# Kernel tuning notes

Hardware: AMD Instinct MI355X
Metric: run time of the kernel (lower is better)

## Reference

```python
import jax, jax.numpy as jnp
import numpy as np

_ANCHORS_PX = np.array([[116,90],[156,198],[373,326],
                        [30,61],[62,45],[59,119],
                        [10,13],[16,30],[33,23]], dtype=np.float32)
IMG = 416.0
NORMD_ANCHORS = jnp.asarray(_ANCHORS_PX / IMG)  # [9,2] normalized (w,h)
CLASSES = 80
LAMBDA_CLASS = 5.0


def _build_targets(targets, F, start):
    # targets: [B,N,5] = (cx,cy,w,h,cls), normalized coords.
    # Vectorized version of the per-box Python loop: IoU-match every box
    # against all 9 anchors (boxes pinned at origin, so IoU = wh overlap),
    # keep boxes whose best anchor belongs to this pyramid level, scatter
    B, N, _ = targets.shape
    C = CLASSES
    cx, cy, w, h = targets[..., 0], targets[..., 1], targets[..., 2], targets[..., 3]
    cls = targets[..., 4].astype(jnp.int32)
    fx, fy = cx * F, cy * F
    gx = jnp.floor(fx).astype(jnp.int32)
    gy = jnp.floor(fy).astype(jnp.int32)
    tx, ty = fx - gx, fy - gy
    aw_all, ah_all = NORMD_ANCHORS[:, 0], NORMD_ANCHORS[:, 1]
    # origin-pinned IoU: inter = min(w,aw)*min(h,ah)
    inter = jnp.minimum(w[..., None], aw_all) * jnp.minimum(h[..., None], ah_all)  # [B,N,9]
    union = (w * h)[..., None] + aw_all * ah_all - inter
    best = jnp.argmax(inter / union, axis=-1)                     # [B,N]
    assigned = (best >= start) & (best < start + 3)
    a = (best % 3).astype(jnp.int32)
    aw = jnp.take(aw_all, best)
    ah = jnp.take(ah_all, best)
    tw = jnp.log(w / aw)
    th = jnp.log(h / ah)
    b = jnp.arange(B, dtype=jnp.int32)[:, None]
    size = B * 3 * F * F
    flat = ((b * 3 + a) * F + gy) * F + gx                        # [B,N]
    flat = jnp.where(assigned, flat, size).reshape(-1)            # OOB -> dropped

    def scat(vals, init=0.0):
        buf = jnp.full((size,), init, dtype=jnp.float32)
        return buf.at[flat].set(vals.reshape(-1), mode='drop').reshape(B, 3, F, F)

    ones = jnp.ones((B, N), jnp.float32)
    t_x, t_y = scat(tx), scat(ty)
    t_w, t_h = scat(tw), scat(th)
    lw_xw, lw_yh = scat(w), scat(h)
    obj = scat(ones)
    noobj = scat(jnp.zeros((B, N), jnp.float32), init=1.0)
    flatc = flat * C + cls.reshape(-1)                            # OOB stays OOB
    cls_t = jnp.zeros((size * C,), jnp.float32).at[flatc].set(1.0, mode='drop')
    cls_t = cls_t.reshape(B, 3, F, F, C)
    return t_x, t_y, t_w, t_h, lw_xw, lw_yh, obj, cls_t, noobj


def _bce_mean(z, t):
    # torch BCELoss(sigmoid(z), t) with default mean reduction, written stably
    return jnp.mean(-(t * jax.nn.log_sigmoid(z) + (1.0 - t) * jax.nn.log_sigmoid(-z)))


def _level_loss(feat, targets, start):
    B, _, F, _ = feat.shape
    C = CLASSES
    t_x, t_y, t_w, t_h, lw_xw, lw_yh, obj, cls_t, noobj = _build_targets(targets, F, start)
    f = feat.reshape(B, 3, 5 + C, F, F).transpose(0, 1, 3, 4, 2)  # [B,3,F,F,5+C]
    zx, zy = f[..., 0], f[..., 1]
    pw, ph = f[..., 2], f[..., 3]
    zc = f[..., 4]
    zcls = f[..., 5:]
    scale = 2.0 - lw_xw * lw_yh
    # NOTE: original multiplies the scalar mean-reduced BCE/MSE by the mask
    # tensor and sums -> scalar_mean * sum(weights). Reproduced faithfully.
    loss_x = _bce_mean(zx, t_x) * jnp.sum(scale * obj)
    loss_y = _bce_mean(zy, t_y) * jnp.sum(scale * obj)
    loss_w = jnp.mean((pw - t_w) ** 2) * jnp.sum(0.5 * scale * obj)
    loss_h = jnp.mean((ph - t_h) ** 2) * jnp.sum(0.5 * scale * obj)
    bce_c = _bce_mean(zc, obj)
    loss_conf = bce_c * jnp.sum(obj) + bce_c * jnp.sum(noobj)     # lambda_obj=lambda_noobj=1
    # class loss: mean BCE over cells where obj==1 (boolean-mask mean in torch)
    bce_cls = -(cls_t * jax.nn.log_sigmoid(zcls) + (1.0 - cls_t) * jax.nn.log_sigmoid(-zcls))
    n_obj = jnp.sum(obj)
    loss_class = jnp.sum(bce_cls * obj[..., None]) / (n_obj * C)
    loss = loss_x + loss_y + loss_w + loss_h + loss_conf + LAMBDA_CLASS * loss_class
    return loss, n_obj


def setup_inputs() -> dict:
    key = jax.random.key(0)
    k1, k2, k3, k4 = jax.random.split(key, 4)
    B, N, C = 64, 50, CLASSES
    p13 = 0.1 * jax.random.normal(k1, (B, 3 * (5 + C), 13, 13), jnp.float32)
    p26 = 0.1 * jax.random.normal(k2, (B, 3 * (5 + C), 26, 26), jnp.float32)
    p52 = 0.1 * jax.random.normal(k3, (B, 3 * (5 + C), 52, 52), jnp.float32)
    kxy, kwh, kc = jax.random.split(k4, 3)
    cxcy = jax.random.uniform(kxy, (B, N, 2), jnp.float32, 0.01, 0.99)
    wh = jax.random.uniform(kwh, (B, N, 2), jnp.float32, 0.02, 0.9)
    cls = jax.random.randint(kc, (B, N, 1), 0, C).astype(jnp.float32)
    targets = jnp.concatenate([cxcy, wh, cls], axis=-1)  # [B,N,5]
    return {"predict_13": p13, "predict_26": p26, "predict_52": p52, "targets": targets}


def reference(predict_13, predict_26, predict_52, targets):
    l13, n13 = _level_loss(predict_13, targets, 0)
    l26, n26 = _level_loss(predict_26, targets, 3)
    l52, n52 = _level_loss(predict_52, targets, 6)
    return (l13 + l26 + l52) / (n13 + n26 + n52)
```

## Files before the change

kernel.cpp:

```cpp
#include <hip/hip_runtime.h>

#define NB 64
#define NT 50
#define NC 80

#define S13 (NB*3*13*13)
#define S26 (NB*3*26*26)
#define S52 (NB*3*52*52)

#define PB_BLOCKS 256
#define DN_BLOCKS 768
#define NBLK (PB_BLOCKS + DN_BLOCKS)

__device__ float g_partT[48][NBLK];

#define A_SPX 0
#define A_SPY 1
#define A_SW2 2
#define A_SH2 3
#define A_SPC 4
#define A_TXZ 5
#define A_TYZ 6
#define A_TW  7
#define A_TH  8
#define A_ZC  9
#define A_SSC 10
#define A_NOB 11
#define A_CSP 12
#define A_CZ  13

__device__ __forceinline__ float softplusf(float z){
    return fmaxf(z, 0.f) + __logf(1.f + __expf(-fabsf(z)));
}

struct TDec {
    int lvl, a, gx, gy, F, FF, off;
    float tx, ty, tw, th, w, h;
    int cls;
};

__device__ __forceinline__ TDec decode_target(const float* __restrict__ tgt, int b, int n){
    const float aw[9] = {116.f/416.f,156.f/416.f,373.f/416.f, 30.f/416.f, 62.f/416.f,
                          59.f/416.f, 10.f/416.f, 16.f/416.f, 33.f/416.f};
    const float ah[9] = { 90.f/416.f,198.f/416.f,326.f/416.f, 61.f/416.f, 45.f/416.f,
                         119.f/416.f, 13.f/416.f, 30.f/416.f, 23.f/416.f};
    const float* t = tgt + (b*NT + n)*5;
    float cx = t[0], cy = t[1], w = t[2], h = t[3];
    TDec d;
    d.cls = (int)t[4];
    d.w = w; d.h = h;
    float wh = w*h;
    int best = 0; float bi = -1.f, baw = aw[0], bah = ah[0];
    #pragma unroll
    for (int k = 0; k < 9; ++k){
        float inter = fminf(w, aw[k]) * fminf(h, ah[k]);
        float uni   = wh + aw[k]*ah[k] - inter;
        float r     = inter / uni;
        if (r > bi){ bi = r; best = k; baw = aw[k]; bah = ah[k]; }
    }
    d.lvl = best / 3;
    d.a   = best - d.lvl*3;
    d.F   = (d.lvl==0) ? 13 : (d.lvl==1 ? 26 : 52);
    d.FF  = d.F * d.F;
    d.off = (d.lvl==0) ? 0 : (d.lvl==1 ? S13 : (S13+S26));
    float fx = cx * (float)d.F, fy = cy * (float)d.F;
    d.gx = (int)floorf(fx); d.gy = (int)floorf(fy);
    d.tx = fx - (float)d.gx; d.ty = fy - (float)d.gy;
    d.tw = logf(w / baw);
    d.th = logf(h / bah);
    return d;
}

template<int FF, int LVL>
__device__ __forceinline__ void dense_scalar(const float* __restrict__ feat, int gb, float* sacc){
    constexpr int elems = NB*3*5*FF;
    constexpr int cFF = 5*FF;
    float s0=0.f,s1=0.f,s2=0.f,s3=0.f,s4=0.f;
    for (int i = gb*256 + (int)threadIdx.x; i < elems; i += DN_BLOCKS*256){
        int ba = i / cFF;
        int r  = i - ba*cFF;
        int c  = r / FF;
        float v = feat[ba*85*FF + r];
        if      (c == 0) s0 += softplusf(v);
        else if (c == 1) s1 += softplusf(v);
        else if (c == 2) s2 += v*v;
        else if (c == 3) s3 += v*v;
        else             s4 += softplusf(v);
    }
    float vals[5] = {s0,s1,s2,s3,s4};
    int lane = threadIdx.x & 63;
    #pragma unroll
    for (int k = 0; k < 5; ++k){
        float v = vals[k];
        #pragma unroll
        for (int o = 32; o > 0; o >>= 1) v += __shfl_down(v, o);
        if (lane == 0) atomicAdd(&sacc[LVL*16 + k], v);
    }
}

template<int FF, int LVL>
__device__ __forceinline__ void dense_vec4(const float* __restrict__ feat, int gb, float* sacc){
    static_assert(FF % 4 == 0, "");
    constexpr int e4   = NB*3*5*FF/4;
    constexpr int cFF4 = 5*FF/4;
    constexpr int qFF  = FF/4;
    const float4* f4 = (const float4*)feat;
    float s0=0.f,s1=0.f,s2=0.f,s3=0.f,s4=0.f;
    for (int i = gb*256 + (int)threadIdx.x; i < e4; i += DN_BLOCKS*256){
        int ba = i / cFF4;
        int r  = i - ba*cFF4;
        int c  = r / qFF;
        float4 v = f4[ba*(85*FF/4) + r];
        if (c == 2 || c == 3){
            float sq = v.x*v.x + v.y*v.y + v.z*v.z + v.w*v.w;
            if (c == 2) s2 += sq; else s3 += sq;
        } else {
            float sp = softplusf(v.x)+softplusf(v.y)+softplusf(v.z)+softplusf(v.w);
            if (c == 0) s0 += sp; else if (c == 1) s1 += sp; else s4 += sp;
        }
    }
    float vals[5] = {s0,s1,s2,s3,s4};
    int lane = threadIdx.x & 63;
    #pragma unroll
    for (int k = 0; k < 5; ++k){
        float v = vals[k];
        #pragma unroll
        for (int o = 32; o > 0; o >>= 1) v += __shfl_down(v, o);
        if (lane == 0) atomicAdd(&sacc[LVL*16 + k], v);
    }
}

__global__ __launch_bounds__(256) void k_fused(const float* __restrict__ p13,
                                              const float* __restrict__ p26,
                                              const float* __restrict__ p52,
                                              const float* __restrict__ tgt){
    __shared__ float sacc[48];
    int tid = threadIdx.x;
    if (tid < 48) sacc[tid] = 0.f;
    __syncthreads();

    if (blockIdx.x < PB_BLOCKS){
        __shared__ int   skey[NT];
        __shared__ int   scb [NT];
        __shared__ int   slvl[NT];
        __shared__ int   scls[NT];
        __shared__ float sf  [NT][6];
        __shared__ unsigned char swin[NT];
        int b = blockIdx.x >> 2, q = blockIdx.x & 3;
        if (tid < NT){
            TDec d = decode_target(tgt, b, tid);
            int flat = ((b*3 + d.a)*d.F + d.gy)*d.F + d.gx;
            skey[tid] = d.off + flat;
            scb [tid] = ((b*3 + d.a)*85)*d.FF + d.gy*d.F + d.gx;
            slvl[tid] = d.lvl; scls[tid] = d.cls;
            sf[tid][0]=d.tx; sf[tid][1]=d.ty; sf[tid][2]=d.tw;
            sf[tid][3]=d.th; sf[tid][4]=d.w;  sf[tid][5]=d.h;
        }
        __syncthreads();
        if (tid < NT){
            int k = skey[tid]; unsigned char wn = 1;
            for (int m = tid+1; m < NT; ++m) if (skey[m] == k){ wn = 0; break; }
            swin[tid] = wn;
        }
        __syncthreads();

        int lane = tid & 63, wv = tid >> 6;
        int n0 = q*13, n1 = (n0+13 < NT) ? n0+13 : NT;
        for (int n = n0 + wv; n < n1; n += 4){
            int lvl = slvl[n];
            const float* feat = (lvl==0) ? p13 : (lvl==1 ? p26 : p52);
            int FF = (lvl==0) ? 169 : (lvl==1 ? 676 : 2704);
            int cb = scb[n];
            int cls = scls[n];
            if (!swin[n]){
                if (lane == 0){
                    float zcl = feat[cb + (5+cls)*FF];
                    atomicAdd(&sacc[lvl*16 + A_CZ], zcl);
                }
                continue;
            }
            float v1 = feat[cb + lane*FF];
            float v2 = (lane < 21) ? feat[cb + (64+lane)*FF] : 0.f;
            float csum = (lane >= 5) ? softplusf(v1) : 0.f;
            if (lane < 21) csum += softplusf(v2);
            #pragma unroll
            for (int o = 32; o > 0; o >>= 1) csum += __shfl_down(csum, o);
            float zx = __shfl(v1, 0), zy = __shfl(v1, 1);
            float pw = __shfl(v1, 2), ph = __shfl(v1, 3), zc = __shfl(v1, 4);
            int ch = 5 + cls;
            float zcl = (ch < 64) ? __shfl(v1, ch) : __shfl(v2, ch - 64);
            if (lane == 0){
                float* acc = &sacc[lvl*16];
                float tx=sf[n][0], ty=sf[n][1], tw=sf[n][2], th=sf[n][3], w=sf[n][4], h=sf[n][5];
                atomicAdd(&acc[A_CZ ], zcl);
                atomicAdd(&acc[A_TXZ], tx*zx);
                atomicAdd(&acc[A_TYZ], ty*zy);
                atomicAdd(&acc[A_TW ], tw*tw - 2.f*pw*tw);
                atomicAdd(&acc[A_TH ], th*th - 2.f*ph*th);
                atomicAdd(&acc[A_ZC ], zc);
                atomicAdd(&acc[A_SSC], 2.f - w*h);
                atomicAdd(&acc[A_NOB], 1.f);
                atomicAdd(&acc[A_CSP], csum);
            }
        }
    } else {
        int gb = blockIdx.x - PB_BLOCKS;
        dense_scalar< 169,0>(p13, gb, sacc);
        dense_vec4  < 676,1>(p26, gb, sacc);
        dense_vec4  <2704,2>(p52, gb, sacc);
    }
    __syncthreads();
    if (tid < 48) g_partT[tid][blockIdx.x] = sacc[tid];
}

__global__ __launch_bounds__(256) void k_final(float* __restrict__ out){
    __shared__ float bins[48];
    int lane = threadIdx.x & 63, wv = threadIdx.x >> 6;
    for (int slot = wv; slot < 48; slot += 4){
        float s = 0.f;
        #pragma unroll
        for (int k = 0; k < NBLK/64; ++k) s += g_partT[slot][k*64 + lane];
        #pragma unroll
        for (int o = 32; o > 0; o >>= 1) s += __shfl_down(s, o);
        if (lane == 0) bins[slot] = s;
    }
    __syncthreads();
    if (threadIdx.x == 0){
        float total = 0.f, ntot = 0.f;
        const int sizes[3] = {S13, S26, S52};
        #pragma unroll
        for (int l = 0; l < 3; ++l){
            const float* a = &bins[l*16];
            float size = (float)sizes[l];
            float ssc  = a[A_SSC];
            float lx = (a[A_SPX] - a[A_TXZ]) / size * ssc;
            float ly = (a[A_SPY] - a[A_TYZ]) / size * ssc;
            float lw = (a[A_SW2] + a[A_TW ]) / size * (0.5f*ssc);
            float lh = (a[A_SH2] + a[A_TH ]) / size * (0.5f*ssc);
            float lc = a[A_SPC] - a[A_ZC];
            float lcls = (a[A_CSP] - a[A_CZ]) / (a[A_NOB]*(float)NC);
            total += lx + ly + lw + lh + lc + 5.f*lcls;
            ntot  += a[A_NOB];
        }
        out[0] = total / ntot;
    }
}

extern "C" void kernel_launch(void* const* d_in, const int* in_sizes, int n_in,
                              void* d_out, int out_size, void* d_ws, size_t ws_size,
                              hipStream_t stream){
    const float* p13 = (const float*)d_in[0];
    const float* p26 = (const float*)d_in[1];
    const float* p52 = (const float*)d_in[2];
    const float* tgt = (const float*)d_in[3];
    float* out = (float*)d_out;

    k_fused<<<NBLK, 256, 0, stream>>>(p13, p26, p52, tgt);
    k_final<<<1, 256, 0, stream>>>(out);
}
```

Baseline: 25.78 us.

## Batch sparse target loads per wave, shrink grid, add polynomial softplus

Each sparse block now handles one whole batch image instead of a quarter, and each wave issues all of its 13 target loads up front into register arrays before reducing them, so memory latency overlaps. The grid shrinks (sparse blocks 256→64, dense blocks 768→448), which cuts the number of partial sums the final kernel reads and sum. Softplus gains a Taylor polynomial for small inputs to avoid exp/log. The trade-offs are higher register pressure, fewer blocks available to hide latency, and a small approximation error near |z|≈0.92.

```diff
diff --git a/kernel.cpp b/kernel.cpp
--- a/kernel.cpp
+++ b/kernel.cpp
@@ -8,9 +8,10 @@
 #define S26 (NB*3*26*26)
 #define S52 (NB*3*52*52)
 
-#define PB_BLOCKS 256
-#define DN_BLOCKS 768
-#define NBLK (PB_BLOCKS + DN_BLOCKS)
+#define SP_BLOCKS 64
+#define DN_BLOCKS 448
+#define NBLK (SP_BLOCKS + DN_BLOCKS)
+#define WPT 13
 
 __device__ float g_partT[48][NBLK];
 
@@ -30,6 +31,10 @@
 #define A_CZ  13
 
 __device__ __forceinline__ float softplusf(float z){
+    float u = z*z;
+    if (fabsf(z) < 0.92f)
+        return 0.6931471805599453f + 0.5f*z
+             + u*(0.125f + u*(-5.2083333e-3f + u*3.4722222e-4f));
     return fmaxf(z, 0.f) + __logf(1.f + __expf(-fabsf(z)));
 }
 
@@ -139,14 +144,14 @@
     if (tid < 48) sacc[tid] = 0.f;
     __syncthreads();
 
-    if (blockIdx.x < PB_BLOCKS){
+    if (blockIdx.x < SP_BLOCKS){
         __shared__ int   skey[NT];
         __shared__ int   scb [NT];
         __shared__ int   slvl[NT];
         __shared__ int   scls[NT];
         __shared__ float sf  [NT][6];
         __shared__ unsigned char swin[NT];
-        int b = blockIdx.x >> 2, q = blockIdx.x & 3;
+        int b = blockIdx.x;
         if (tid < NT){
             TDec d = decode_target(tgt, b, tid);
             int flat = ((b*3 + d.a)*d.F + d.gy)*d.F + d.gx;
@@ -165,30 +170,44 @@
         __syncthreads();
 
         int lane = tid & 63, wv = tid >> 6;
-        int n0 = q*13, n1 = (n0+13 < NT) ? n0+13 : NT;
-        for (int n = n0 + wv; n < n1; n += 4){
+        int base = wv * WPT;
+
+        float v1s[WPT], v2s[WPT];
+        #pragma unroll
+        for (int k = 0; k < WPT; ++k){
+            int n = base + k;
+            v1s[k] = 0.f; v2s[k] = 0.f;
+            if (n < NT){
+                int lvl = slvl[n];
+                const float* feat = (lvl==0) ? p13 : (lvl==1 ? p26 : p52);
+                int FF = (lvl==0) ? 169 : (lvl==1 ? 676 : 2704);
+                int cb = scb[n];
+                if (swin[n]){
+                    v1s[k] = feat[cb + lane*FF];
+                    if (lane < 21) v2s[k] = feat[cb + (64+lane)*FF];
+                } else if (lane == 0){
+                    v1s[k] = feat[cb + (5+scls[n])*FF];
+                }
+            }
+        }
+
+        #pragma unroll
+        for (int k = 0; k < WPT; ++k){
+            int n = base + k;
+            if (n >= NT) continue;
             int lvl = slvl[n];
-            const float* feat = (lvl==0) ? p13 : (lvl==1 ? p26 : p52);
-            int FF = (lvl==0) ? 169 : (lvl==1 ? 676 : 2704);
-            int cb = scb[n];
-            int cls = scls[n];
             if (!swin[n]){
-                if (lane == 0){
-                    float zcl = feat[cb + (5+cls)*FF];
-                    atomicAdd(&sacc[lvl*16 + A_CZ], zcl);
-                }
+                if (lane == 0) atomicAdd(&sacc[lvl*16 + A_CZ], v1s[k]);
                 continue;
             }
-            float v1 = feat[cb + lane*FF];
-            float v2 = (lane < 21) ? feat[cb + (64+lane)*FF] : 0.f;
-            float csum = (lane >= 5) ? softplusf(v1) : 0.f;
-            if (lane < 21) csum += softplusf(v2);
+            float csum = (lane >= 5) ? softplusf(v1s[k]) : 0.f;
+            if (lane < 21) csum += softplusf(v2s[k]);
             #pragma unroll
             for (int o = 32; o > 0; o >>= 1) csum += __shfl_down(csum, o);
-            float zx = __shfl(v1, 0), zy = __shfl(v1, 1);
-            float pw = __shfl(v1, 2), ph = __shfl(v1, 3), zc = __shfl(v1, 4);
-            int ch = 5 + cls;
-            float zcl = (ch < 64) ? __shfl(v1, ch) : __shfl(v2, ch - 64);
+            float zx = __shfl(v1s[k], 0), zy = __shfl(v1s[k], 1);
+            float pw = __shfl(v1s[k], 2), ph = __shfl(v1s[k], 3), zc = __shfl(v1s[k], 4);
+            int ch = 5 + scls[n];
+            float zcl = (ch < 64) ? __shfl(v1s[k], ch) : __shfl(v2s[k], ch - 64);
             if (lane == 0){
                 float* acc = &sacc[lvl*16];
                 float tx=sf[n][0], ty=sf[n][1], tw=sf[n][2], th=sf[n][3], w=sf[n][4], h=sf[n][5];
@@ -204,7 +223,7 @@
             }
         }
     } else {
-        int gb = blockIdx.x - PB_BLOCKS;
+        int gb = blockIdx.x - SP_BLOCKS;
         dense_scalar< 169,0>(p13, gb, sacc);
         dense_vec4  < 676,1>(p26, gb, sacc);
         dense_vec4  <2704,2>(p52, gb, sacc);
```

Result: slower. 33.81 us (+31.2%).
